# Kernel optimization log

Measured on AMD Instinct MI355X. Metric: run time of the kernel, lower is better.

Reference implementation:

```python
import jax, jax.numpy as jnp
import numpy as np

N = 50000
E = 800000
F_IN = 128
H1, C1 = 8, 8          # conv1: 8 heads x 8 channels -> 64
H2, C2 = 1, 64         # conv2: 1 head x num_classes=64
E_TEST = 100000
NEG_SLOPE = 0.2


def setup_inputs() -> dict:
    key = jax.random.key(0)
    ks = jax.random.split(key, 12)
    x = jax.random.normal(ks[0], (N, F_IN), dtype=jnp.float32)
    edge_index = jax.random.randint(ks[1], (2, E), 0, N, dtype=jnp.int64)
    test_pos_edge_index = jax.random.randint(ks[2], (2, E_TEST), 0, N, dtype=jnp.int64)
    test_neg_edge_index = jax.random.randint(ks[3], (2, E_TEST), 0, N, dtype=jnp.int64)
    s1 = 1.0 / np.sqrt(F_IN)
    s2 = 1.0 / np.sqrt(H1 * C1)
    W1 = jax.random.normal(ks[4], (F_IN, H1 * C1), dtype=jnp.float32) * s1
    att_src1 = jax.random.normal(ks[5], (H1, C1), dtype=jnp.float32) * s2
    att_dst1 = jax.random.normal(ks[6], (H1, C1), dtype=jnp.float32) * s2
    bias1 = jnp.zeros((H1 * C1,), dtype=jnp.float32)
    W2 = jax.random.normal(ks[7], (H1 * C1, H2 * C2), dtype=jnp.float32) * s2
    att_src2 = jax.random.normal(ks[8], (H2, C2), dtype=jnp.float32) * (1.0 / np.sqrt(C2))
    att_dst2 = jax.random.normal(ks[9], (H2, C2), dtype=jnp.float32) * (1.0 / np.sqrt(C2))
    bias2 = jnp.zeros((H2 * C2,), dtype=jnp.float32)
    return {"x": x, "edge_index": edge_index,
            "test_pos_edge_index": test_pos_edge_index,
            "test_neg_edge_index": test_neg_edge_index,
            "W1": W1, "att_src1": att_src1, "att_dst1": att_dst1, "bias1": bias1,
            "W2": W2, "att_src2": att_src2, "att_dst2": att_dst2, "bias2": bias2}


def gat_conv(x, edge_index, W, att_src, att_dst, bias, heads, out_ch):
    # x: [N, F]; edge_index: [2, E'] with self-loops already added (src -> dst)
    n = x.shape[0]
    h = (x @ W).reshape(n, heads, out_ch)              # [N, H, C]
    a_src = jnp.einsum('nhc,hc->nh', h, att_src)       # [N, H]
    a_dst = jnp.einsum('nhc,hc->nh', h, att_dst)       # [N, H]
    src, dst = edge_index[0], edge_index[1]
    alpha = jax.nn.leaky_relu(a_src[src] + a_dst[dst], NEG_SLOPE)  # [E', H]
    m = jax.ops.segment_max(alpha, dst, num_segments=n)            # per-dst max
    m = jnp.where(jnp.isfinite(m), m, 0.0)
    e = jnp.exp(alpha - m[dst])
    denom = jax.ops.segment_sum(e, dst, num_segments=n)
    coef = e / jnp.maximum(denom[dst], 1e-16)                      # [E', H]
    msg = h[src] * coef[:, :, None]                                # [E', H, C]
    out = jax.ops.segment_sum(msg, dst, num_segments=n)            # [N, H, C]
    return out.reshape(n, heads * out_ch) + bias


def reference(x, edge_index, test_pos_edge_index, test_neg_edge_index,
              W1, att_src1, att_dst1, bias1, W2, att_src2, att_dst2, bias2):
    # add self-loops (PyG GATConv default)
    loops = jnp.arange(N, dtype=edge_index.dtype)
    ei = jnp.concatenate([edge_index, jnp.stack([loops, loops])], axis=1)
    z = gat_conv(x, ei, W1, att_src1, att_dst1, bias1, H1, C1)
    z = jax.nn.elu(z)
    z = gat_conv(z, ei, W2, att_src2, att_dst2, bias2, H2, C2)   # [N, 64]
    e = jnp.concatenate([test_pos_edge_index, test_neg_edge_index], axis=-1)
    logits = (z[e[0]] * z[e[1]]).sum(axis=-1)                    # [2*E_TEST]
    return logits
```

## Files before the change

kernel.cpp:

```cpp
#include <hip/hip_runtime.h>
#include <math.h>

#define NN 50000
#define FIN 128
#define EE 800000
#define ETEST 100000
#define NEG_SLOPE 0.2f
#define NB 196
#define BB 256
#define EPB 3125
#define M  (NB * BB)
#define MB 196
#define XP 68

static inline int cdiv(long long a, int b) { return (int)((a + b - 1) / b); }


__global__ void count_kernel(const int* __restrict__ ei, int* __restrict__ cnt) {
    __shared__ int hist[NB];
    int tid = threadIdx.x, blk = blockIdx.x;
    for (int i = tid; i < NB; i += 256) hist[i] = 0;
    __syncthreads();
    int beg = blk * EPB, end = beg + EPB; if (end > EE) end = EE;
    for (int e = beg + tid; e < end; e += 256)
        atomicAdd(&hist[((unsigned)ei[EE + e]) >> 8], 1);
    __syncthreads();
    for (int b = tid; b < NB; b += 256) cnt[b * BB + blk] = hist[b];
}

__global__ void block_sums(const int* __restrict__ cnt, int* __restrict__ bsum) {
    int idx = blockIdx.x * 256 + threadIdx.x;
    int v = cnt[idx];
#pragma unroll
    for (int off = 32; off >= 1; off >>= 1) v += __shfl_xor(v, off, 64);
    __shared__ int ws[4];
    if ((threadIdx.x & 63) == 0) ws[threadIdx.x >> 6] = v;
    __syncthreads();
    if (threadIdx.x == 0) bsum[blockIdx.x] = ws[0] + ws[1] + ws[2] + ws[3];
}

__global__ void scan_bsums(const int* __restrict__ bsum, int* __restrict__ boff) {
    __shared__ int s[256];
    int t = threadIdx.x;
    int v = (t < MB) ? bsum[t] : 0;
    s[t] = v;
    __syncthreads();
#pragma unroll
    for (int off = 1; off < 256; off <<= 1) {
        int u = (t >= off) ? s[t - off] : 0;
        __syncthreads();
        s[t] += u;
        __syncthreads();
    }
    if (t < MB) boff[t] = s[t] - v;
}

__global__ void scan_final(const int* __restrict__ cnt, const int* __restrict__ boff,
                           int* __restrict__ off) {
    __shared__ int s[256];
    int t = threadIdx.x;
    int idx = blockIdx.x * 256 + t;
    int v = cnt[idx];
    s[t] = v;
    __syncthreads();
#pragma unroll
    for (int off2 = 1; off2 < 256; off2 <<= 1) {
        int u = (t >= off2) ? s[t - off2] : 0;
        __syncthreads();
        s[t] += u;
        __syncthreads();
    }
    off[idx] = boff[blockIdx.x] + s[t] - v;
}

__global__ void bin_kernel(const int* __restrict__ ei, const int* __restrict__ off,
                           unsigned* __restrict__ binned) {
    __shared__ int cur[NB];
    int tid = threadIdx.x, blk = blockIdx.x;
    for (int b = tid; b < NB; b += 256) cur[b] = off[b * BB + blk];
    __syncthreads();
    int beg = blk * EPB, end = beg + EPB; if (end > EE) end = EE;
    for (int e = beg + tid; e < end; e += 256) {
        unsigned dst = (unsigned)ei[EE + e], src = (unsigned)ei[e];
        int b = dst >> 8;
        int r = atomicAdd(&cur[b], 1);
        binned[r] = (dst << 16) | src;
    }
}

__global__ void csr_kernel(const unsigned* __restrict__ binned, const int* __restrict__ off,
                           int* __restrict__ rowptr, int* __restrict__ col) {
    __shared__ int cnt[256], s[256], cur[256];
    int b = blockIdx.x, t = threadIdx.x;
    int start = off[b * BB];
    int end = (b + 1 < NB) ? off[(b + 1) * BB] : EE;
    cnt[t] = 0;
    __syncthreads();
    for (int i = start + t; i < end; i += 256)
        atomicAdd(&cnt[(binned[i] >> 16) & 255], 1);
    __syncthreads();
    int v = cnt[t];
    s[t] = v;
    __syncthreads();
#pragma unroll
    for (int off2 = 1; off2 < 256; off2 <<= 1) {
        int u = (t >= off2) ? s[t - off2] : 0;
        __syncthreads();
        s[t] += u;
        __syncthreads();
    }
    int excl = start + s[t] - v;
    int dst = b * 256 + t;
    if (dst < NN) rowptr[dst] = excl;
    if (b == NB - 1 && t == 0) rowptr[NN] = EE;
    cur[t] = excl;
    __syncthreads();
    for (int i = start + t; i < end; i += 256) {
        unsigned p = binned[i];
        int dl = (p >> 16) & 255;
        int r = atomicAdd(&cur[dl], 1);
        col[r] = (int)(p & 0xFFFFu);
    }
}


__global__ void __launch_bounds__(256) gemm1_kernel(
        const float* __restrict__ x, const float* __restrict__ W,
        const float* __restrict__ att_src, const float* __restrict__ att_dst,
        float* __restrict__ h, float* __restrict__ a_src, float* __restrict__ a_dst) {
    __shared__ __align__(16) float Ws[FIN * 64];
    __shared__ __align__(16) float xs[32 * XP];
    int tid = threadIdx.x;
    for (int i = tid; i < FIN * 64 / 4; i += 256)
        ((float4*)Ws)[i] = ((const float4*)W)[i];
    int B = blockIdx.x * 64;
    int wave = tid >> 6, lane = tid & 63;
    int rg = lane >> 4, cg = lane & 15;
    int rbase = wave * 16 + rg * 4;
    float acc[4][4] = {};
    for (int kc = 0; kc < FIN; kc += 32) {
        __syncthreads();
#pragma unroll
        for (int p = 0; p < 2; ++p) {
            int idx = p * 256 + tid;
            int r = idx >> 3;
            int m = idx & 7;
            int row = B + r;
            float4 v = (row < NN) ? ((const float4*)(x + (size_t)row * FIN + kc))[m]
                                  : make_float4(0.f, 0.f, 0.f, 0.f);
            int c4 = m << 2;
            xs[(c4 + 0) * XP + r] = v.x;
            xs[(c4 + 1) * XP + r] = v.y;
            xs[(c4 + 2) * XP + r] = v.z;
            xs[(c4 + 3) * XP + r] = v.w;
        }
        __syncthreads();
#pragma unroll 4
        for (int k = 0; k < 32; ++k) {
            float4 w4 = *(const float4*)&Ws[(kc + k) * 64 + cg * 4];
            float4 x4 = *(const float4*)&xs[k * XP + rbase];
            acc[0][0] = fmaf(x4.x, w4.x, acc[0][0]); acc[0][1] = fmaf(x4.x, w4.y, acc[0][1]);
            acc[0][2] = fmaf(x4.x, w4.z, acc[0][2]); acc[0][3] = fmaf(x4.x, w4.w, acc[0][3]);
            acc[1][0] = fmaf(x4.y, w4.x, acc[1][0]); acc[1][1] = fmaf(x4.y, w4.y, acc[1][1]);
            acc[1][2] = fmaf(x4.y, w4.z, acc[1][2]); acc[1][3] = fmaf(x4.y, w4.w, acc[1][3]);
            acc[2][0] = fmaf(x4.z, w4.x, acc[2][0]); acc[2][1] = fmaf(x4.z, w4.y, acc[2][1]);
            acc[2][2] = fmaf(x4.z, w4.z, acc[2][2]); acc[2][3] = fmaf(x4.z, w4.w, acc[2][3]);
            acc[3][0] = fmaf(x4.w, w4.x, acc[3][0]); acc[3][1] = fmaf(x4.w, w4.y, acc[3][1]);
            acc[3][2] = fmaf(x4.w, w4.z, acc[3][2]); acc[3][3] = fmaf(x4.w, w4.w, acc[3][3]);
        }
    }
    float as0 = att_src[4 * cg + 0], as1 = att_src[4 * cg + 1],
          as2 = att_src[4 * cg + 2], as3 = att_src[4 * cg + 3];
    float ad0 = att_dst[4 * cg + 0], ad1 = att_dst[4 * cg + 1],
          ad2 = att_dst[4 * cg + 2], ad3 = att_dst[4 * cg + 3];
#pragma unroll
    for (int j = 0; j < 4; ++j) {
        int row = B + rbase + j;
        if (row >= NN) continue;
        float4 hv = make_float4(acc[j][0], acc[j][1], acc[j][2], acc[j][3]);
        *(float4*)(h + (size_t)row * 64 + cg * 4) = hv;
        float ps = fmaf(hv.x, as0, fmaf(hv.y, as1, fmaf(hv.z, as2, hv.w * as3)));
        float pd = fmaf(hv.x, ad0, fmaf(hv.y, ad1, fmaf(hv.z, ad2, hv.w * ad3)));
        ps += __shfl_xor(ps, 1, 64);
        pd += __shfl_xor(pd, 1, 64);
        if ((cg & 1) == 0) {
            a_src[row * 8 + (cg >> 1)] = ps;
            a_dst[row * 8 + (cg >> 1)] = pd;
        }
    }
}

__global__ void __launch_bounds__(256) gemm2_kernel(
        const float* __restrict__ z, const float* __restrict__ W,
        const float* __restrict__ att_src, const float* __restrict__ att_dst,
        float* __restrict__ h, float* __restrict__ a_src, float* __restrict__ a_dst) {
    __shared__ __align__(16) float Ws[64 * 64];
    __shared__ __align__(16) float xs[64 * XP];
    int tid = threadIdx.x;
    for (int i = tid; i < 64 * 64 / 4; i += 256)
        ((float4*)Ws)[i] = ((const float4*)W)[i];
    int B = blockIdx.x * 64;
#pragma unroll
    for (int p = 0; p < 4; ++p) {
        int idx = p * 256 + tid;
        int r = idx >> 4;
        int m = idx & 15;
        int row = B + r;
        float4 v = (row < NN) ? ((const float4*)(z + (size_t)row * 64))[m]
                              : make_float4(0.f, 0.f, 0.f, 0.f);
        int c4 = m << 2;
        xs[(c4 + 0) * XP + r] = v.x;
        xs[(c4 + 1) * XP + r] = v.y;
        xs[(c4 + 2) * XP + r] = v.z;
        xs[(c4 + 3) * XP + r] = v.w;
    }
    int wave = tid >> 6, lane = tid & 63;
    int rg = lane >> 4, cg = lane & 15;
    int rbase = wave * 16 + rg * 4;
    float acc[4][4] = {};
    __syncthreads();
#pragma unroll 4
    for (int k = 0; k < 64; ++k) {
        float4 w4 = *(const float4*)&Ws[k * 64 + cg * 4];
        float4 x4 = *(const float4*)&xs[k * XP + rbase];
        acc[0][0] = fmaf(x4.x, w4.x, acc[0][0]); acc[0][1] = fmaf(x4.x, w4.y, acc[0][1]);
        acc[0][2] = fmaf(x4.x, w4.z, acc[0][2]); acc[0][3] = fmaf(x4.x, w4.w, acc[0][3]);
        acc[1][0] = fmaf(x4.y, w4.x, acc[1][0]); acc[1][1] = fmaf(x4.y, w4.y, acc[1][1]);
        acc[1][2] = fmaf(x4.y, w4.z, acc[1][2]); acc[1][3] = fmaf(x4.y, w4.w, acc[1][3]);
        acc[2][0] = fmaf(x4.z, w4.x, acc[2][0]); acc[2][1] = fmaf(x4.z, w4.y, acc[2][1]);
        acc[2][2] = fmaf(x4.z, w4.z, acc[2][2]); acc[2][3] = fmaf(x4.z, w4.w, acc[2][3]);
        acc[3][0] = fmaf(x4.w, w4.x, acc[3][0]); acc[3][1] = fmaf(x4.w, w4.y, acc[3][1]);
        acc[3][2] = fmaf(x4.w, w4.z, acc[3][2]); acc[3][3] = fmaf(x4.w, w4.w, acc[3][3]);
    }
    float as0 = att_src[4 * cg + 0], as1 = att_src[4 * cg + 1],
          as2 = att_src[4 * cg + 2], as3 = att_src[4 * cg + 3];
    float ad0 = att_dst[4 * cg + 0], ad1 = att_dst[4 * cg + 1],
          ad2 = att_dst[4 * cg + 2], ad3 = att_dst[4 * cg + 3];
#pragma unroll
    for (int j = 0; j < 4; ++j) {
        int row = B + rbase + j;
        if (row >= NN) continue;
        float4 hv = make_float4(acc[j][0], acc[j][1], acc[j][2], acc[j][3]);
        *(float4*)(h + (size_t)row * 64 + cg * 4) = hv;
        float ps = fmaf(hv.x, as0, fmaf(hv.y, as1, fmaf(hv.z, as2, hv.w * as3)));
        float pd = fmaf(hv.x, ad0, fmaf(hv.y, ad1, fmaf(hv.z, ad2, hv.w * ad3)));
#pragma unroll
        for (int off = 8; off >= 1; off >>= 1) {
            ps += __shfl_xor(ps, off, 64);
            pd += __shfl_xor(pd, off, 64);
        }
        if (cg == 0) { a_src[row] = ps; a_dst[row] = pd; }
    }
}


__global__ void gat1_gather(const int* __restrict__ rowptr, const int* __restrict__ col,
                            const float* __restrict__ asrc, const float* __restrict__ adst,
                            const float* __restrict__ hfeat, const float* __restrict__ bias,
                            float* __restrict__ z1) {
    int v = blockIdx.x * 4 + (threadIdx.x >> 6);
    if (v >= NN) return;
    int lane = threadIdx.x & 63;
    int j = lane >> 3;
    int hh = lane & 7;
    int beg = rowptr[v], end = rowptr[v + 1];
    float ad_a = adst[v * 8 + hh];
    float aself = asrc[v * 8 + j] + adst[v * 8 + j];
    float eself = __expf(fmaxf(aself, NEG_SLOPE * aself));
    float acc = eself * hfeat[(size_t)v * 64 + lane];
    float den_a = 0.f;
    for (int i = beg; i < end; i += 8) {
        int lim = end - i;
        int idx = (j < lim) ? i + j : end - 1;
        int vs = col[idx];
        float a = asrc[vs * 8 + hh] + ad_a;
        float e = __expf(fmaxf(a, NEG_SLOPE * a));
        e = (j < lim) ? e : 0.f;
        den_a += e;
#pragma unroll
        for (int u = 0; u < 8; ++u) {
            int s_u = __builtin_amdgcn_readlane(vs, u * 8);
            float eb = __shfl(e, u * 8 + j, 64);
            float f = hfeat[(size_t)s_u * 64 + lane];
            acc = fmaf(eb, f, acc);
        }
    }
    den_a += __shfl_xor(den_a, 8, 64);
    den_a += __shfl_xor(den_a, 16, 64);
    den_a += __shfl_xor(den_a, 32, 64);
    float den = __shfl(den_a, j, 64) + eself;
    float o = acc / fmaxf(den, 1e-16f) + bias[lane];
    z1[(size_t)v * 64 + lane] = o > 0.f ? o : expm1f(o);
}

__global__ void gat2_gather(const int* __restrict__ rowptr, const int* __restrict__ col,
                            const float* __restrict__ asrc, const float* __restrict__ adst,
                            const float* __restrict__ hfeat, const float* __restrict__ bias,
                            float* __restrict__ z2) {
    int v = blockIdx.x * 4 + (threadIdx.x >> 6);
    if (v >= NN) return;
    int lane = threadIdx.x & 63;
    int j16 = lane & 15;
    int beg = rowptr[v], end = rowptr[v + 1];
    float ad = adst[v];
    float aself = asrc[v] + ad;
    float eself = __expf(fmaxf(aself, NEG_SLOPE * aself));
    float den = eself;
    float acc = eself * hfeat[(size_t)v * 64 + lane];
    for (int i = beg; i < end; i += 16) {
        int lim = end - i;
        int idx = (j16 < lim) ? i + j16 : end - 1;
        int vs = col[idx];
        float a = asrc[vs] + ad;
        float e = __expf(fmaxf(a, NEG_SLOPE * a));
        e = (j16 < lim) ? e : 0.f;
#pragma unroll
        for (int u = 0; u < 16; ++u) {
            int s_u = __builtin_amdgcn_readlane(vs, u);
            float e_u = __int_as_float(__builtin_amdgcn_readlane(__float_as_int(e), u));
            float f = hfeat[(size_t)s_u * 64 + lane];
            den += e_u;
            acc = fmaf(e_u, f, acc);
        }
    }
    z2[(size_t)v * 64 + lane] = acc / fmaxf(den, 1e-16f) + bias[lane];
}

__global__ void logits_kernel(const int* __restrict__ pos, const int* __restrict__ neg,
                              const float* __restrict__ z2, float* __restrict__ out) {
    int t = blockIdx.x * 256 + threadIdx.x;
    int i = t >> 4;
    if (i >= 2 * ETEST) return;
    int sub = t & 15;
    int a, b;
    if (i < ETEST) { a = pos[i]; b = pos[ETEST + i]; }
    else           { a = neg[i - ETEST]; b = neg[i]; }
    float4 va = ((const float4*)(z2 + (size_t)a * 64))[sub];
    float4 vb = ((const float4*)(z2 + (size_t)b * 64))[sub];
    float p = fmaf(va.x, vb.x, fmaf(va.y, vb.y, fmaf(va.z, vb.z, va.w * vb.w)));
#pragma unroll
    for (int off = 8; off >= 1; off >>= 1) p += __shfl_xor(p, off, 64);
    if (sub == 0) out[i] = p;
}

extern "C" void kernel_launch(void* const* d_in, const int* in_sizes, int n_in,
                              void* d_out, int out_size, void* d_ws, size_t ws_size,
                              hipStream_t stream) {
    const float* x    = (const float*)d_in[0];
    const int*   ei   = (const int*)d_in[1];
    const int*   pos  = (const int*)d_in[2];
    const int*   neg  = (const int*)d_in[3];
    const float* W1   = (const float*)d_in[4];
    const float* asr1 = (const float*)d_in[5];
    const float* ads1 = (const float*)d_in[6];
    const float* b1   = (const float*)d_in[7];
    const float* W2   = (const float*)d_in[8];
    const float* asr2 = (const float*)d_in[9];
    const float* ads2 = (const float*)d_in[10];
    const float* b2   = (const float*)d_in[11];
    float* out = (float*)d_out;

    float* ws  = (float*)d_ws;
    float* h1  = ws;
    float* z1  = h1 + (size_t)NN * 64;
    float* z2  = z1 + (size_t)NN * 64;
    float* as1 = z2 + (size_t)NN * 64;
    float* ad1 = as1 + (size_t)NN * 8;
    float* as2 = ad1 + (size_t)NN * 8;
    float* ad2 = as2 + NN;
    int* cnt    = (int*)(ad2 + NN);
    int* off    = cnt + M;
    int* bsum   = off + M;
    int* boff   = bsum + MB;
    int* rowptr = boff + MB;
    unsigned* binned = (unsigned*)(rowptr + NN + 1);
    int* csrcol = (int*)(binned + EE);

    count_kernel<<<BB, 256, 0, stream>>>(ei, cnt);
    block_sums<<<MB, 256, 0, stream>>>(cnt, bsum);
    scan_bsums<<<1, 256, 0, stream>>>(bsum, boff);
    scan_final<<<MB, 256, 0, stream>>>(cnt, boff, off);
    bin_kernel<<<BB, 256, 0, stream>>>(ei, off, binned);
    csr_kernel<<<NB, 256, 0, stream>>>(binned, off, rowptr, csrcol);

    gemm1_kernel<<<cdiv(NN, 64), 256, 0, stream>>>(x, W1, asr1, ads1, h1, as1, ad1);
    gat1_gather<<<cdiv(NN, 4), 256, 0, stream>>>(rowptr, csrcol, as1, ad1, h1, b1, z1);

    gemm2_kernel<<<cdiv(NN, 64), 256, 0, stream>>>(z1, W2, asr2, ads2, h1, as2, ad2);
    gat2_gather<<<cdiv(NN, 4), 256, 0, stream>>>(rowptr, csrcol, as2, ad2, h1, b2, z2);

    logits_kernel<<<cdiv((long long)2 * ETEST * 16, 256), 256, 0, stream>>>(pos, neg, z2, out);
}
```

Baseline: 234.6 us.

## Fuse layer-1 aggregation with layer-2 linear transform and widen logits loads

New measurement: 256.8 us. 1.09x slower.

```diff
diff --git a/kernel.cpp b/kernel.cpp
--- a/kernel.cpp
+++ b/kernel.cpp
@@ -190,107 +190,70 @@
     }
 }
 
-__global__ void __launch_bounds__(256) gemm2_kernel(
-        const float* __restrict__ z, const float* __restrict__ W,
-        const float* __restrict__ att_src, const float* __restrict__ att_dst,
-        float* __restrict__ h, float* __restrict__ a_src, float* __restrict__ a_dst) {
-    __shared__ __align__(16) float Ws[64 * 64];
-    __shared__ __align__(16) float xs[64 * XP];
+__global__ void __launch_bounds__(256) gat1_fused(
+        const int* __restrict__ rowptr, const int* __restrict__ col,
+        const float* __restrict__ asrc, const float* __restrict__ adst,
+        const float* __restrict__ hfeat, const float* __restrict__ bias1,
+        const float* __restrict__ W2, const float* __restrict__ att_src2,
+        const float* __restrict__ att_dst2,
+        float* __restrict__ h2, float* __restrict__ as2, float* __restrict__ ad2) {
+    __shared__ __align__(16) float W2s[64 * 64];
     int tid = threadIdx.x;
     for (int i = tid; i < 64 * 64 / 4; i += 256)
-        ((float4*)Ws)[i] = ((const float4*)W)[i];
-    int B = blockIdx.x * 64;
-#pragma unroll
-    for (int p = 0; p < 4; ++p) {
-        int idx = p * 256 + tid;
-        int r = idx >> 4;
-        int m = idx & 15;
-        int row = B + r;
-        float4 v = (row < NN) ? ((const float4*)(z + (size_t)row * 64))[m]
-                              : make_float4(0.f, 0.f, 0.f, 0.f);
-        int c4 = m << 2;
-        xs[(c4 + 0) * XP + r] = v.x;
-        xs[(c4 + 1) * XP + r] = v.y;
-        xs[(c4 + 2) * XP + r] = v.z;
-        xs[(c4 + 3) * XP + r] = v.w;
-    }
-    int wave = tid >> 6, lane = tid & 63;
-    int rg = lane >> 4, cg = lane & 15;
-    int rbase = wave * 16 + rg * 4;
-    float acc[4][4] = {};
-    __syncthreads();
-#pragma unroll 4
-    for (int k = 0; k < 64; ++k) {
-        float4 w4 = *(const float4*)&Ws[k * 64 + cg * 4];
-        float4 x4 = *(const float4*)&xs[k * XP + rbase];
-        acc[0][0] = fmaf(x4.x, w4.x, acc[0][0]); acc[0][1] = fmaf(x4.x, w4.y, acc[0][1]);
-        acc[0][2] = fmaf(x4.x, w4.z, acc[0][2]); acc[0][3] = fmaf(x4.x, w4.w, acc[0][3]);
-        acc[1][0] = fmaf(x4.y, w4.x, acc[1][0]); acc[1][1] = fmaf(x4.y, w4.y, acc[1][1]);
-        acc[1][2] = fmaf(x4.y, w4.z, acc[1][2]); acc[1][3] = fmaf(x4.y, w4.w, acc[1][3]);
-        acc[2][0] = fmaf(x4.z, w4.x, acc[2][0]); acc[2][1] = fmaf(x4.z, w4.y, acc[2][1]);
-        acc[2][2] = fmaf(x4.z, w4.z, acc[2][2]); acc[2][3] = fmaf(x4.z, w4.w, acc[2][3]);
-        acc[3][0] = fmaf(x4.w, w4.x, acc[3][0]); acc[3][1] = fmaf(x4.w, w4.y, acc[3][1]);
-        acc[3][2] = fmaf(x4.w, w4.z, acc[3][2]); acc[3][3] = fmaf(x4.w, w4.w, acc[3][3]);
-    }
-    float as0 = att_src[4 * cg + 0], as1 = att_src[4 * cg + 1],
-          as2 = att_src[4 * cg + 2], as3 = att_src[4 * cg + 3];
-    float ad0 = att_dst[4 * cg + 0], ad1 = att_dst[4 * cg + 1],
-          ad2 = att_dst[4 * cg + 2], ad3 = att_dst[4 * cg + 3];
-#pragma unroll
-    for (int j = 0; j < 4; ++j) {
-        int row = B + rbase + j;
-        if (row >= NN) continue;
-        float4 hv = make_float4(acc[j][0], acc[j][1], acc[j][2], acc[j][3]);
-        *(float4*)(h + (size_t)row * 64 + cg * 4) = hv;
-        float ps = fmaf(hv.x, as0, fmaf(hv.y, as1, fmaf(hv.z, as2, hv.w * as3)));
-        float pd = fmaf(hv.x, ad0, fmaf(hv.y, ad1, fmaf(hv.z, ad2, hv.w * ad3)));
-#pragma unroll
-        for (int off = 8; off >= 1; off >>= 1) {
+        ((float4*)W2s)[i] = ((const float4*)W2)[i];
+    __syncthreads();
+    int lane = tid & 63, wv = tid >> 6;
+    int j = lane >> 3;
+    int hh = lane & 7;
+    float b1v = bias1[lane];
+    float at_s = att_src2[lane], at_d = att_dst2[lane];
+    int v0 = blockIdx.x * 16 + wv * 4;
+#pragma unroll
+    for (int it = 0; it < 4; ++it) {
+        int v = v0 + it;
+        int beg = rowptr[v], end = rowptr[v + 1];
+        float ad_a = adst[v * 8 + hh];
+        float aself = asrc[v * 8 + j] + adst[v * 8 + j];
+        float eself = __expf(fmaxf(aself, NEG_SLOPE * aself));
+        float acc = eself * hfeat[(size_t)v * 64 + lane];
+        float den_a = 0.f;
+        for (int i = beg; i < end; i += 8) {
+            int lim = end - i;
+            int idx = (j < lim) ? i + j : end - 1;
+            int vs = col[idx];
+            float a = asrc[vs * 8 + hh] + ad_a;
+            float e = __expf(fmaxf(a, NEG_SLOPE * a));
+            e = (j < lim) ? e : 0.f;
+            den_a += e;
+#pragma unroll
+            for (int u = 0; u < 8; ++u) {
+                int s_u = __builtin_amdgcn_readlane(vs, u * 8);
+                float eb = __shfl(e, u * 8 + j, 64);
+                float f = hfeat[(size_t)s_u * 64 + lane];
+                acc = fmaf(eb, f, acc);
+            }
+        }
+        den_a += __shfl_xor(den_a, 8, 64);
+        den_a += __shfl_xor(den_a, 16, 64);
+        den_a += __shfl_xor(den_a, 32, 64);
+        float den = __shfl(den_a, j, 64) + eself;
+        float o = acc / fmaxf(den, 1e-16f) + b1v;
+        float z = o > 0.f ? o : expm1f(o);
+        float hv = 0.f;
+#pragma unroll 16
+        for (int k = 0; k < 64; ++k) {
+            float zk = __shfl(z, k, 64);
+            hv = fmaf(zk, W2s[k * 64 + lane], hv);
+        }
+        h2[(size_t)v * 64 + lane] = hv;
+        float ps = hv * at_s, pd = hv * at_d;
+#pragma unroll
+        for (int off = 32; off >= 1; off >>= 1) {
             ps += __shfl_xor(ps, off, 64);
             pd += __shfl_xor(pd, off, 64);
         }
-        if (cg == 0) { a_src[row] = ps; a_dst[row] = pd; }
-    }
-}
-
-
-__global__ void gat1_gather(const int* __restrict__ rowptr, const int* __restrict__ col,
-                            const float* __restrict__ asrc, const float* __restrict__ adst,
-                            const float* __restrict__ hfeat, const float* __restrict__ bias,
-                            float* __restrict__ z1) {
-    int v = blockIdx.x * 4 + (threadIdx.x >> 6);
-    if (v >= NN) return;
-    int lane = threadIdx.x & 63;
-    int j = lane >> 3;
-    int hh = lane & 7;
-    int beg = rowptr[v], end = rowptr[v + 1];
-    float ad_a = adst[v * 8 + hh];
-    float aself = asrc[v * 8 + j] + adst[v * 8 + j];
-    float eself = __expf(fmaxf(aself, NEG_SLOPE * aself));
-    float acc = eself * hfeat[(size_t)v * 64 + lane];
-    float den_a = 0.f;
-    for (int i = beg; i < end; i += 8) {
-        int lim = end - i;
-        int idx = (j < lim) ? i + j : end - 1;
-        int vs = col[idx];
-        float a = asrc[vs * 8 + hh] + ad_a;
-        float e = __expf(fmaxf(a, NEG_SLOPE * a));
-        e = (j < lim) ? e : 0.f;
-        den_a += e;
-#pragma unroll
-        for (int u = 0; u < 8; ++u) {
-            int s_u = __builtin_amdgcn_readlane(vs, u * 8);
-            float eb = __shfl(e, u * 8 + j, 64);
-            float f = hfeat[(size_t)s_u * 64 + lane];
-            acc = fmaf(eb, f, acc);
-        }
-    }
-    den_a += __shfl_xor(den_a, 8, 64);
-    den_a += __shfl_xor(den_a, 16, 64);
-    den_a += __shfl_xor(den_a, 32, 64);
-    float den = __shfl(den_a, j, 64) + eself;
-    float o = acc / fmaxf(den, 1e-16f) + bias[lane];
-    z1[(size_t)v * 64 + lane] = o > 0.f ? o : expm1f(o);
+        if (lane == 0) { as2[v] = ps; ad2[v] = pd; }
+    }
 }
 
 __global__ void gat2_gather(const int* __restrict__ rowptr, const int* __restrict__ col,
@@ -329,17 +292,20 @@
 __global__ void logits_kernel(const int* __restrict__ pos, const int* __restrict__ neg,
                               const float* __restrict__ z2, float* __restrict__ out) {
     int t = blockIdx.x * 256 + threadIdx.x;
-    int i = t >> 4;
+    int i = t >> 3;
     if (i >= 2 * ETEST) return;
-    int sub = t & 15;
+    int sub = t & 7;
     int a, b;
     if (i < ETEST) { a = pos[i]; b = pos[ETEST + i]; }
     else           { a = neg[i - ETEST]; b = neg[i]; }
-    float4 va = ((const float4*)(z2 + (size_t)a * 64))[sub];
-    float4 vb = ((const float4*)(z2 + (size_t)b * 64))[sub];
-    float p = fmaf(va.x, vb.x, fmaf(va.y, vb.y, fmaf(va.z, vb.z, va.w * vb.w)));
-#pragma unroll
-    for (int off = 8; off >= 1; off >>= 1) p += __shfl_xor(p, off, 64);
+    const float4* pa = (const float4*)(z2 + (size_t)a * 64) + sub * 2;
+    const float4* pb = (const float4*)(z2 + (size_t)b * 64) + sub * 2;
+    float4 va0 = pa[0], va1 = pa[1];
+    float4 vb0 = pb[0], vb1 = pb[1];
+    float p = fmaf(va0.x, vb0.x, fmaf(va0.y, vb0.y, fmaf(va0.z, vb0.z, va0.w * vb0.w)));
+    p = fmaf(va1.x, vb1.x, fmaf(va1.y, vb1.y, fmaf(va1.z, vb1.z, fmaf(va1.w, vb1.w, p))));
+#pragma unroll
+    for (int off = 4; off >= 1; off >>= 1) p += __shfl_xor(p, off, 64);
     if (sub == 0) out[i] = p;
 }
 
@@ -362,8 +328,8 @@
 
     float* ws  = (float*)d_ws;
     float* h1  = ws;
-    float* z1  = h1 + (size_t)NN * 64;
-    float* z2  = z1 + (size_t)NN * 64;
+    float* h2  = h1 + (size_t)NN * 64;
+    float* z2  = h2 + (size_t)NN * 64;
     float* as1 = z2 + (size_t)NN * 64;
     float* ad1 = as1 + (size_t)NN * 8;
     float* as2 = ad1 + (size_t)NN * 8;
@@ -384,10 +350,10 @@
     csr_kernel<<<NB, 256, 0, stream>>>(binned, off, rowptr, csrcol);
 
     gemm1_kernel<<<cdiv(NN, 64), 256, 0, stream>>>(x, W1, asr1, ads1, h1, as1, ad1);
-    gat1_gather<<<cdiv(NN, 4), 256, 0, stream>>>(rowptr, csrcol, as1, ad1, h1, b1, z1);
-
-    gemm2_kernel<<<cdiv(NN, 64), 256, 0, stream>>>(z1, W2, asr2, ads2, h1, as2, ad2);
-    gat2_gather<<<cdiv(NN, 4), 256, 0, stream>>>(rowptr, csrcol, as2, ad2, h1, b2, z2);
-
-    logits_kernel<<<cdiv((long long)2 * ETEST * 16, 256), 256, 0, stream>>>(pos, neg, z2, out);
-}
+    gat1_fused<<<3125, 256, 0, stream>>>(rowptr, csrcol, as1, ad1, h1, b1,
+                                         W2, asr2, ads2, h2, as2, ad2);
+
+    gat2_gather<<<cdiv(NN, 4), 256, 0, stream>>>(rowptr, csrcol, as2, ad2, h2, b2, z2);
+
+    logits_kernel<<<cdiv((long long)2 * ETEST * 8, 256), 256, 0, stream>>>(pos, neg, z2, out);
+}
```

## Fuse CSR construction kernels into one cooperative kernel with grid syncs

Applied to the files above, without the earlier changes.

Result: slower. 369.1 us (+57.4%).

```diff
diff --git a/kernel.cpp b/kernel.cpp
--- a/kernel.cpp
+++ b/kernel.cpp
@@ -1,5 +1,8 @@
 #include <hip/hip_runtime.h>
+#include <hip/hip_cooperative_groups.h>
 #include <math.h>
+
+namespace cg = cooperative_groups;
 
 #define NN 50000
 #define FIN 128
@@ -15,111 +18,96 @@
 
 static inline int cdiv(long long a, int b) { return (int)((a + b - 1) / b); }
 
-
-__global__ void count_kernel(const int* __restrict__ ei, int* __restrict__ cnt) {
-    __shared__ int hist[NB];
-    int tid = threadIdx.x, blk = blockIdx.x;
-    for (int i = tid; i < NB; i += 256) hist[i] = 0;
+__global__ void __launch_bounds__(256) csr_build(
+        const int* __restrict__ ei, int* __restrict__ cnt, int* __restrict__ bsum,
+        int* __restrict__ boff, int* __restrict__ offl, int* __restrict__ rowptr,
+        unsigned* __restrict__ binned, int* __restrict__ col) {
+    cg::grid_group grid = cg::this_grid();
+    __shared__ int sh[768];
+    int blk = blockIdx.x, t = threadIdx.x;
+    int beg = blk * EPB, end = beg + EPB; if (end > EE) end = EE;
+
+    for (int i = t; i < NB; i += 256) sh[i] = 0;
     __syncthreads();
-    int beg = blk * EPB, end = beg + EPB; if (end > EE) end = EE;
-    for (int e = beg + tid; e < end; e += 256)
-        atomicAdd(&hist[((unsigned)ei[EE + e]) >> 8], 1);
+    for (int e = beg + t; e < end; e += 256)
+        atomicAdd(&sh[((unsigned)ei[EE + e]) >> 8], 1);
     __syncthreads();
-    for (int b = tid; b < NB; b += 256) cnt[b * BB + blk] = hist[b];
-}
-
-__global__ void block_sums(const int* __restrict__ cnt, int* __restrict__ bsum) {
-    int idx = blockIdx.x * 256 + threadIdx.x;
-    int v = cnt[idx];
-#pragma unroll
-    for (int off = 32; off >= 1; off >>= 1) v += __shfl_xor(v, off, 64);
-    __shared__ int ws[4];
-    if ((threadIdx.x & 63) == 0) ws[threadIdx.x >> 6] = v;
+    for (int b = t; b < NB; b += 256) cnt[b * BB + blk] = sh[b];
+    grid.sync();
+
+    if (blk < MB) {
+        int idx = blk * 256 + t;
+        int v = cnt[idx];
+        sh[t] = v;
+        __syncthreads();
+        for (int o = 1; o < 256; o <<= 1) {
+            int u = (t >= o) ? sh[t - o] : 0;
+            __syncthreads();
+            sh[t] += u;
+            __syncthreads();
+        }
+        offl[idx] = sh[t] - v;
+        if (t == 255) bsum[blk] = sh[255];
+    }
+    grid.sync();
+
+    if (blk == 0) {
+        int v = (t < MB) ? bsum[t] : 0;
+        sh[t] = v;
+        __syncthreads();
+        for (int o = 1; o < 256; o <<= 1) {
+            int u = (t >= o) ? sh[t - o] : 0;
+            __syncthreads();
+            sh[t] += u;
+            __syncthreads();
+        }
+        if (t < MB) boff[t] = sh[t] - v;
+    }
+    grid.sync();
+
+    for (int b = t; b < NB; b += 256) sh[b] = offl[b * BB + blk] + boff[b];
     __syncthreads();
-    if (threadIdx.x == 0) bsum[blockIdx.x] = ws[0] + ws[1] + ws[2] + ws[3];
-}
-
-__global__ void scan_bsums(const int* __restrict__ bsum, int* __restrict__ boff) {
-    __shared__ int s[256];
-    int t = threadIdx.x;
-    int v = (t < MB) ? bsum[t] : 0;
-    s[t] = v;
-    __syncthreads();
-#pragma unroll
-    for (int off = 1; off < 256; off <<= 1) {
-        int u = (t >= off) ? s[t - off] : 0;
-        __syncthreads();
-        s[t] += u;
-        __syncthreads();
-    }
-    if (t < MB) boff[t] = s[t] - v;
-}
-
-__global__ void scan_final(const int* __restrict__ cnt, const int* __restrict__ boff,
-                           int* __restrict__ off) {
-    __shared__ int s[256];
-    int t = threadIdx.x;
-    int idx = blockIdx.x * 256 + t;
-    int v = cnt[idx];
-    s[t] = v;
-    __syncthreads();
-#pragma unroll
-    for (int off2 = 1; off2 < 256; off2 <<= 1) {
-        int u = (t >= off2) ? s[t - off2] : 0;
-        __syncthreads();
-        s[t] += u;
-        __syncthreads();
-    }
-    off[idx] = boff[blockIdx.x] + s[t] - v;
-}
-
-__global__ void bin_kernel(const int* __restrict__ ei, const int* __restrict__ off,
-                           unsigned* __restrict__ binned) {
-    __shared__ int cur[NB];
-    int tid = threadIdx.x, blk = blockIdx.x;
-    for (int b = tid; b < NB; b += 256) cur[b] = off[b * BB + blk];
-    __syncthreads();
-    int beg = blk * EPB, end = beg + EPB; if (end > EE) end = EE;
-    for (int e = beg + tid; e < end; e += 256) {
+    for (int e = beg + t; e < end; e += 256) {
         unsigned dst = (unsigned)ei[EE + e], src = (unsigned)ei[e];
         int b = dst >> 8;
-        int r = atomicAdd(&cur[b], 1);
+        int r = atomicAdd(&sh[b], 1);
         binned[r] = (dst << 16) | src;
     }
-}
-
-__global__ void csr_kernel(const unsigned* __restrict__ binned, const int* __restrict__ off,
-                           int* __restrict__ rowptr, int* __restrict__ col) {
-    __shared__ int cnt[256], s[256], cur[256];
-    int b = blockIdx.x, t = threadIdx.x;
-    int start = off[b * BB];
-    int end = (b + 1 < NB) ? off[(b + 1) * BB] : EE;
-    cnt[t] = 0;
-    __syncthreads();
-    for (int i = start + t; i < end; i += 256)
-        atomicAdd(&cnt[(binned[i] >> 16) & 255], 1);
-    __syncthreads();
-    int v = cnt[t];
-    s[t] = v;
-    __syncthreads();
-#pragma unroll
-    for (int off2 = 1; off2 < 256; off2 <<= 1) {
-        int u = (t >= off2) ? s[t - off2] : 0;
-        __syncthreads();
-        s[t] += u;
-        __syncthreads();
-    }
-    int excl = start + s[t] - v;
-    int dst = b * 256 + t;
-    if (dst < NN) rowptr[dst] = excl;
-    if (b == NB - 1 && t == 0) rowptr[NN] = EE;
-    cur[t] = excl;
-    __syncthreads();
-    for (int i = start + t; i < end; i += 256) {
-        unsigned p = binned[i];
-        int dl = (p >> 16) & 255;
-        int r = atomicAdd(&cur[dl], 1);
-        col[r] = (int)(p & 0xFFFFu);
+    grid.sync();
+
+    if (blk < NB) {
+        int* dcnt = sh;
+        int* ds   = sh + 256;
+        int* dcur = sh + 512;
+        int b = blk;
+        int start = offl[b * BB] + boff[b];
+        int bend = (b + 1 < NB) ? (offl[(b + 1) * BB] + boff[b + 1]) : EE;
+        dcnt[t] = 0;
+        __syncthreads();
+        for (int i = start + t; i < bend; i += 256)
+            atomicAdd(&dcnt[(binned[i] >> 16) & 255], 1);
+        __syncthreads();
+        int v = dcnt[t];
+        ds[t] = v;
+        __syncthreads();
+        for (int o = 1; o < 256; o <<= 1) {
+            int u = (t >= o) ? ds[t - o] : 0;
+            __syncthreads();
+            ds[t] += u;
+            __syncthreads();
+        }
+        int excl = start + ds[t] - v;
+        int dst = b * 256 + t;
+        if (dst < NN) rowptr[dst] = excl;
+        if (b == NB - 1 && t == 0) rowptr[NN] = EE;
+        dcur[t] = excl;
+        __syncthreads();
+        for (int i = start + t; i < bend; i += 256) {
+            unsigned p = binned[i];
+            int dl = (p >> 16) & 255;
+            int r = atomicAdd(&dcur[dl], 1);
+            col[r] = (int)(p & 0xFFFFu);
+        }
     }
 }
 
@@ -135,7 +123,7 @@
         ((float4*)Ws)[i] = ((const float4*)W)[i];
     int B = blockIdx.x * 64;
     int wave = tid >> 6, lane = tid & 63;
-    int rg = lane >> 4, cg = lane & 15;
+    int rg = lane >> 4, cg2 = lane & 15;
     int rbase = wave * 16 + rg * 4;
     float acc[4][4] = {};
     for (int kc = 0; kc < FIN; kc += 32) {
@@ -157,7 +145,7 @@
         __syncthreads();
 #pragma unroll 4
         for (int k = 0; k < 32; ++k) {
-            float4 w4 = *(const float4*)&Ws[(kc + k) * 64 + cg * 4];
+            float4 w4 = *(const float4*)&Ws[(kc + k) * 64 + cg2 * 4];
             float4 x4 = *(const float4*)&xs[k * XP + rbase];
             acc[0][0] = fmaf(x4.x, w4.x, acc[0][0]); acc[0][1] = fmaf(x4.x, w4.y, acc[0][1]);
             acc[0][2] = fmaf(x4.x, w4.z, acc[0][2]); acc[0][3] = fmaf(x4.x, w4.w, acc[0][3]);
@@ -169,23 +157,23 @@
             acc[3][2] = fmaf(x4.w, w4.z, acc[3][2]); acc[3][3] = fmaf(x4.w, w4.w, acc[3][3]);
         }
     }
-    float as0 = att_src[4 * cg + 0], as1 = att_src[4 * cg + 1],
-          as2 = att_src[4 * cg + 2], as3 = att_src[4 * cg + 3];
-    float ad0 = att_dst[4 * cg + 0], ad1 = att_dst[4 * cg + 1],
-          ad2 = att_dst[4 * cg + 2], ad3 = att_dst[4 * cg + 3];
+    float as0 = att_src[4 * cg2 + 0], as1 = att_src[4 * cg2 + 1],
+          as2 = att_src[4 * cg2 + 2], as3 = att_src[4 * cg2 + 3];
+    float ad0 = att_dst[4 * cg2 + 0], ad1 = att_dst[4 * cg2 + 1],
+          ad2 = att_dst[4 * cg2 + 2], ad3 = att_dst[4 * cg2 + 3];
 #pragma unroll
     for (int j = 0; j < 4; ++j) {
         int row = B + rbase + j;
         if (row >= NN) continue;
         float4 hv = make_float4(acc[j][0], acc[j][1], acc[j][2], acc[j][3]);
-        *(float4*)(h + (size_t)row * 64 + cg * 4) = hv;
+        *(float4*)(h + (size_t)row * 64 + cg2 * 4) = hv;
         float ps = fmaf(hv.x, as0, fmaf(hv.y, as1, fmaf(hv.z, as2, hv.w * as3)));
         float pd = fmaf(hv.x, ad0, fmaf(hv.y, ad1, fmaf(hv.z, ad2, hv.w * ad3)));
         ps += __shfl_xor(ps, 1, 64);
         pd += __shfl_xor(pd, 1, 64);
-        if ((cg & 1) == 0) {
-            a_src[row * 8 + (cg >> 1)] = ps;
-            a_dst[row * 8 + (cg >> 1)] = pd;
+        if ((cg2 & 1) == 0) {
+            a_src[row * 8 + (cg2 >> 1)] = ps;
+            a_dst[row * 8 + (cg2 >> 1)] = pd;
         }
     }
 }
@@ -215,13 +203,13 @@
         xs[(c4 + 3) * XP + r] = v.w;
     }
     int wave = tid >> 6, lane = tid & 63;
-    int rg = lane >> 4, cg = lane & 15;
+    int rg = lane >> 4, cg2 = lane & 15;
     int rbase = wave * 16 + rg * 4;
     float acc[4][4] = {};
     __syncthreads();
 #pragma unroll 4
     for (int k = 0; k < 64; ++k) {
-        float4 w4 = *(const float4*)&Ws[k * 64 + cg * 4];
+        float4 w4 = *(const float4*)&Ws[k * 64 + cg2 * 4];
         float4 x4 = *(const float4*)&xs[k * XP + rbase];
         acc[0][0] = fmaf(x4.x, w4.x, acc[0][0]); acc[0][1] = fmaf(x4.x, w4.y, acc[0][1]);
         acc[0][2] = fmaf(x4.x, w4.z, acc[0][2]); acc[0][3] = fmaf(x4.x, w4.w, acc[0][3]);
@@ -232,16 +220,16 @@
         acc[3][0] = fmaf(x4.w, w4.x, acc[3][0]); acc[3][1] = fmaf(x4.w, w4.y, acc[3][1]);
         acc[3][2] = fmaf(x4.w, w4.z, acc[3][2]); acc[3][3] = fmaf(x4.w, w4.w, acc[3][3]);
     }
-    float as0 = att_src[4 * cg + 0], as1 = att_src[4 * cg + 1],
-          as2 = att_src[4 * cg + 2], as3 = att_src[4 * cg + 3];
-    float ad0 = att_dst[4 * cg + 0], ad1 = att_dst[4 * cg + 1],
-          ad2 = att_dst[4 * cg + 2], ad3 = att_dst[4 * cg + 3];
+    float as0 = att_src[4 * cg2 + 0], as1 = att_src[4 * cg2 + 1],
+          as2 = att_src[4 * cg2 + 2], as3 = att_src[4 * cg2 + 3];
+    float ad0 = att_dst[4 * cg2 + 0], ad1 = att_dst[4 * cg2 + 1],
+          ad2 = att_dst[4 * cg2 + 2], ad3 = att_dst[4 * cg2 + 3];
 #pragma unroll
     for (int j = 0; j < 4; ++j) {
         int row = B + rbase + j;
         if (row >= NN) continue;
         float4 hv = make_float4(acc[j][0], acc[j][1], acc[j][2], acc[j][3]);
-        *(float4*)(h + (size_t)row * 64 + cg * 4) = hv;
+        *(float4*)(h + (size_t)row * 64 + cg2 * 4) = hv;
         float ps = fmaf(hv.x, as0, fmaf(hv.y, as1, fmaf(hv.z, as2, hv.w * as3)));
         float pd = fmaf(hv.x, ad0, fmaf(hv.y, ad1, fmaf(hv.z, ad2, hv.w * ad3)));
 #pragma unroll
@@ -249,7 +237,7 @@
             ps += __shfl_xor(ps, off, 64);
             pd += __shfl_xor(pd, off, 64);
         }
-        if (cg == 0) { a_src[row] = ps; a_dst[row] = pd; }
+        if (cg2 == 0) { a_src[row] = ps; a_dst[row] = pd; }
     }
 }
 
@@ -360,8 +348,8 @@
     const float* b2   = (const float*)d_in[11];
     float* out = (float*)d_out;
 
-    float* ws  = (float*)d_ws;
-    float* h1  = ws;
+    float* wsp = (float*)d_ws;
+    float* h1  = wsp;
     float* z1  = h1 + (size_t)NN * 64;
     float* z2  = z1 + (size_t)NN * 64;
     float* as1 = z2 + (size_t)NN * 64;
@@ -369,19 +357,16 @@
     float* as2 = ad1 + (size_t)NN * 8;
     float* ad2 = as2 + NN;
     int* cnt    = (int*)(ad2 + NN);
-    int* off    = cnt + M;
-    int* bsum   = off + M;
+    int* offl   = cnt + M;
+    int* bsum   = offl + M;
     int* boff   = bsum + MB;
     int* rowptr = boff + MB;
     unsigned* binned = (unsigned*)(rowptr + NN + 1);
     int* csrcol = (int*)(binned + EE);
 
-    count_kernel<<<BB, 256, 0, stream>>>(ei, cnt);
-    block_sums<<<MB, 256, 0, stream>>>(cnt, bsum);
-    scan_bsums<<<1, 256, 0, stream>>>(bsum, boff);
-    scan_final<<<MB, 256, 0, stream>>>(cnt, boff, off);
-    bin_kernel<<<BB, 256, 0, stream>>>(ei, off, binned);
-    csr_kernel<<<NB, 256, 0, stream>>>(binned, off, rowptr, csrcol);
+    void* cargs[] = {(void*)&ei, (void*)&cnt, (void*)&bsum, (void*)&boff,
+                     (void*)&offl, (void*)&rowptr, (void*)&binned, (void*)&csrcol};
+    hipLaunchCooperativeKernel((void*)csr_build, dim3(BB), dim3(256), cargs, 0, stream);
 
     gemm1_kernel<<<cdiv(NN, 64), 256, 0, stream>>>(x, W1, asr1, ads1, h1, as1, ad1);
     gat1_gather<<<cdiv(NN, 4), 256, 0, stream>>>(rowptr, csrcol, as1, ad1, h1, b1, z1);
```

## Replace count-scan CSR build with fixed-capacity buckets and atomic reservation

Applied to the files above, without the earlier changes.

Result: no change. 231.7 us (-1.2%).

```diff
diff --git a/kernel.cpp b/kernel.cpp
--- a/kernel.cpp
+++ b/kernel.cpp
@@ -9,113 +9,75 @@
 #define NB 196
 #define BB 256
 #define EPB 3125
-#define M  (NB * BB)
-#define MB 196
+#define BSTRIDE 5120
 #define XP 68
 
 static inline int cdiv(long long a, int b) { return (int)((a + b - 1) / b); }
 
 
-__global__ void count_kernel(const int* __restrict__ ei, int* __restrict__ cnt) {
+__global__ void init_gcur(int* __restrict__ gcur) {
+    int t = threadIdx.x;
+    if (t < NB) gcur[t] = t * BSTRIDE;
+}
+
+__global__ void __launch_bounds__(256) bin_kernel(const int* __restrict__ ei,
+                                                  int* __restrict__ gcur,
+                                                  unsigned* __restrict__ binned) {
     __shared__ int hist[NB];
-    int tid = threadIdx.x, blk = blockIdx.x;
-    for (int i = tid; i < NB; i += 256) hist[i] = 0;
+    int t = threadIdx.x, blk = blockIdx.x;
+    for (int b = t; b < NB; b += 256) hist[b] = 0;
     __syncthreads();
     int beg = blk * EPB, end = beg + EPB; if (end > EE) end = EE;
-    for (int e = beg + tid; e < end; e += 256)
-        atomicAdd(&hist[((unsigned)ei[EE + e]) >> 8], 1);
-    __syncthreads();
-    for (int b = tid; b < NB; b += 256) cnt[b * BB + blk] = hist[b];
-}
-
-__global__ void block_sums(const int* __restrict__ cnt, int* __restrict__ bsum) {
-    int idx = blockIdx.x * 256 + threadIdx.x;
-    int v = cnt[idx];
-#pragma unroll
-    for (int off = 32; off >= 1; off >>= 1) v += __shfl_xor(v, off, 64);
-    __shared__ int ws[4];
-    if ((threadIdx.x & 63) == 0) ws[threadIdx.x >> 6] = v;
-    __syncthreads();
-    if (threadIdx.x == 0) bsum[blockIdx.x] = ws[0] + ws[1] + ws[2] + ws[3];
-}
-
-__global__ void scan_bsums(const int* __restrict__ bsum, int* __restrict__ boff) {
-    __shared__ int s[256];
-    int t = threadIdx.x;
-    int v = (t < MB) ? bsum[t] : 0;
+    unsigned pk[13];
+    int n = 0;
+    for (int e = beg + t; e < end; e += 256) {
+        unsigned dst = (unsigned)ei[EE + e], src = (unsigned)ei[e];
+        unsigned p = (dst << 16) | src;
+        pk[n++] = p;
+        atomicAdd(&hist[p >> 24], 1);
+    }
+    __syncthreads();
+    for (int b = t; b < NB; b += 256) {
+        int c = hist[b];
+        if (c > 0) hist[b] = atomicAdd(&gcur[b], c);
+    }
+    __syncthreads();
+    for (int i = 0; i < n; ++i) {
+        unsigned p = pk[i];
+        int r = atomicAdd(&hist[p >> 24], 1);
+        binned[r] = p;
+    }
+}
+
+__global__ void __launch_bounds__(256) csr_kernel(const unsigned* __restrict__ binned,
+                                                  const int* __restrict__ gcur,
+                                                  int* __restrict__ begA, int* __restrict__ endA,
+                                                  int* __restrict__ col) {
+    __shared__ int cnt[256], s[256], cur[256];
+    int b = blockIdx.x, t = threadIdx.x;
+    int start = b * BSTRIDE;
+    int bend = gcur[b];
+    cnt[t] = 0;
+    __syncthreads();
+    for (int i = start + t; i < bend; i += 256)
+        atomicAdd(&cnt[(binned[i] >> 16) & 255], 1);
+    __syncthreads();
+    int v = cnt[t];
     s[t] = v;
     __syncthreads();
 #pragma unroll
-    for (int off = 1; off < 256; off <<= 1) {
-        int u = (t >= off) ? s[t - off] : 0;
+    for (int o = 1; o < 256; o <<= 1) {
+        int u = (t >= o) ? s[t - o] : 0;
         __syncthreads();
         s[t] += u;
         __syncthreads();
     }
-    if (t < MB) boff[t] = s[t] - v;
-}
-
-__global__ void scan_final(const int* __restrict__ cnt, const int* __restrict__ boff,
-                           int* __restrict__ off) {
-    __shared__ int s[256];
-    int t = threadIdx.x;
-    int idx = blockIdx.x * 256 + t;
-    int v = cnt[idx];
-    s[t] = v;
-    __syncthreads();
-#pragma unroll
-    for (int off2 = 1; off2 < 256; off2 <<= 1) {
-        int u = (t >= off2) ? s[t - off2] : 0;
-        __syncthreads();
-        s[t] += u;
-        __syncthreads();
-    }
-    off[idx] = boff[blockIdx.x] + s[t] - v;
-}
-
-__global__ void bin_kernel(const int* __restrict__ ei, const int* __restrict__ off,
-                           unsigned* __restrict__ binned) {
-    __shared__ int cur[NB];
-    int tid = threadIdx.x, blk = blockIdx.x;
-    for (int b = tid; b < NB; b += 256) cur[b] = off[b * BB + blk];
-    __syncthreads();
-    int beg = blk * EPB, end = beg + EPB; if (end > EE) end = EE;
-    for (int e = beg + tid; e < end; e += 256) {
-        unsigned dst = (unsigned)ei[EE + e], src = (unsigned)ei[e];
-        int b = dst >> 8;
-        int r = atomicAdd(&cur[b], 1);
-        binned[r] = (dst << 16) | src;
-    }
-}
-
-__global__ void csr_kernel(const unsigned* __restrict__ binned, const int* __restrict__ off,
-                           int* __restrict__ rowptr, int* __restrict__ col) {
-    __shared__ int cnt[256], s[256], cur[256];
-    int b = blockIdx.x, t = threadIdx.x;
-    int start = off[b * BB];
-    int end = (b + 1 < NB) ? off[(b + 1) * BB] : EE;
-    cnt[t] = 0;
-    __syncthreads();
-    for (int i = start + t; i < end; i += 256)
-        atomicAdd(&cnt[(binned[i] >> 16) & 255], 1);
-    __syncthreads();
-    int v = cnt[t];
-    s[t] = v;
-    __syncthreads();
-#pragma unroll
-    for (int off2 = 1; off2 < 256; off2 <<= 1) {
-        int u = (t >= off2) ? s[t - off2] : 0;
-        __syncthreads();
-        s[t] += u;
-        __syncthreads();
-    }
     int excl = start + s[t] - v;
     int dst = b * 256 + t;
-    if (dst < NN) rowptr[dst] = excl;
-    if (b == NB - 1 && t == 0) rowptr[NN] = EE;
+    if (dst < NN) { begA[dst] = excl; endA[dst] = excl + v; }
     cur[t] = excl;
     __syncthreads();
-    for (int i = start + t; i < end; i += 256) {
+    for (int i = start + t; i < bend; i += 256) {
         unsigned p = binned[i];
         int dl = (p >> 16) & 255;
         int r = atomicAdd(&cur[dl], 1);
@@ -254,7 +216,8 @@
 }
 
 
-__global__ void gat1_gather(const int* __restrict__ rowptr, const int* __restrict__ col,
+__global__ void gat1_gather(const int* __restrict__ begA, const int* __restrict__ endA,
+                            const int* __restrict__ col,
                             const float* __restrict__ asrc, const float* __restrict__ adst,
                             const float* __restrict__ hfeat, const float* __restrict__ bias,
                             float* __restrict__ z1) {
@@ -263,7 +226,7 @@
     int lane = threadIdx.x & 63;
     int j = lane >> 3;
     int hh = lane & 7;
-    int beg = rowptr[v], end = rowptr[v + 1];
+    int beg = begA[v], end = endA[v];
     float ad_a = adst[v * 8 + hh];
     float aself = asrc[v * 8 + j] + adst[v * 8 + j];
     float eself = __expf(fmaxf(aself, NEG_SLOPE * aself));
@@ -293,7 +256,8 @@
     z1[(size_t)v * 64 + lane] = o > 0.f ? o : expm1f(o);
 }
 
-__global__ void gat2_gather(const int* __restrict__ rowptr, const int* __restrict__ col,
+__global__ void gat2_gather(const int* __restrict__ begA, const int* __restrict__ endA,
+                            const int* __restrict__ col,
                             const float* __restrict__ asrc, const float* __restrict__ adst,
                             const float* __restrict__ hfeat, const float* __restrict__ bias,
                             float* __restrict__ z2) {
@@ -301,7 +265,7 @@
     if (v >= NN) return;
     int lane = threadIdx.x & 63;
     int j16 = lane & 15;
-    int beg = rowptr[v], end = rowptr[v + 1];
+    int beg = begA[v], end = endA[v];
     float ad = adst[v];
     float aself = asrc[v] + ad;
     float eself = __expf(fmaxf(aself, NEG_SLOPE * aself));
@@ -360,34 +324,29 @@
     const float* b2   = (const float*)d_in[11];
     float* out = (float*)d_out;
 
-    float* ws  = (float*)d_ws;
-    float* h1  = ws;
+    float* wsp = (float*)d_ws;
+    float* h1  = wsp;
     float* z1  = h1 + (size_t)NN * 64;
     float* z2  = z1 + (size_t)NN * 64;
     float* as1 = z2 + (size_t)NN * 64;
     float* ad1 = as1 + (size_t)NN * 8;
     float* as2 = ad1 + (size_t)NN * 8;
     float* ad2 = as2 + NN;
-    int* cnt    = (int*)(ad2 + NN);
-    int* off    = cnt + M;
-    int* bsum   = off + M;
-    int* boff   = bsum + MB;
-    int* rowptr = boff + MB;
-    unsigned* binned = (unsigned*)(rowptr + NN + 1);
-    int* csrcol = (int*)(binned + EE);
-
-    count_kernel<<<BB, 256, 0, stream>>>(ei, cnt);
-    block_sums<<<MB, 256, 0, stream>>>(cnt, bsum);
-    scan_bsums<<<1, 256, 0, stream>>>(bsum, boff);
-    scan_final<<<MB, 256, 0, stream>>>(cnt, boff, off);
-    bin_kernel<<<BB, 256, 0, stream>>>(ei, off, binned);
-    csr_kernel<<<NB, 256, 0, stream>>>(binned, off, rowptr, csrcol);
+    int* gcur   = (int*)(ad2 + NN);
+    int* begA   = gcur + NB;
+    int* endA   = begA + NN;
+    unsigned* binned = (unsigned*)(endA + NN);
+    int* csrcol = (int*)(binned + (size_t)NB * BSTRIDE);
+
+    init_gcur<<<1, 256, 0, stream>>>(gcur);
+    bin_kernel<<<BB, 256, 0, stream>>>(ei, gcur, binned);
+    csr_kernel<<<NB, 256, 0, stream>>>(binned, gcur, begA, endA, csrcol);
 
     gemm1_kernel<<<cdiv(NN, 64), 256, 0, stream>>>(x, W1, asr1, ads1, h1, as1, ad1);
-    gat1_gather<<<cdiv(NN, 4), 256, 0, stream>>>(rowptr, csrcol, as1, ad1, h1, b1, z1);
+    gat1_gather<<<cdiv(NN, 4), 256, 0, stream>>>(begA, endA, csrcol, as1, ad1, h1, b1, z1);
 
     gemm2_kernel<<<cdiv(NN, 64), 256, 0, stream>>>(z1, W2, asr2, ads2, h1, as2, ad2);
-    gat2_gather<<<cdiv(NN, 4), 256, 0, stream>>>(rowptr, csrcol, as2, ad2, h1, b2, z2);
+    gat2_gather<<<cdiv(NN, 4), 256, 0, stream>>>(begA, endA, csrcol, as2, ad2, h1, b2, z2);
 
     logits_kernel<<<cdiv((long long)2 * ETEST * 16, 256), 256, 0, stream>>>(pos, neg, z2, out);
 }
```
